# Performance work log

Hardware: AMD Instinct MI355X
Metric: run time of the kernel (lower is better)

## Reference

```python
import jax, jax.numpy as jnp
import numpy as np
from jax import lax

SEQ, B, F, L = 32, 32, 64, 256
OC = 128          # out_channels
K = 5
PAD = (K - 1) // 2
GROUPS = 4 * OC // 32  # GroupNorm groups = 16
EPS = 1e-5


def group_norm(x, w, b):
    # x: (B, C, L); normalize over each group's (C//G, L) slice
    bsz, c, l = x.shape
    xg = x.reshape(bsz, GROUPS, -1)
    mu = jnp.mean(xg, axis=-1, keepdims=True)
    var = jnp.var(xg, axis=-1, keepdims=True)
    xg = (xg - mu) * lax.rsqrt(var + EPS)
    return xg.reshape(bsz, c, l) * w[None, :, None] + b[None, :, None]


def setup_inputs() -> dict:
    key = jax.random.key(0)
    k1, k2, k3 = jax.random.split(key, 3)
    fan_in = (F + OC) * K
    return {
        "inputs": jax.random.normal(k1, (SEQ, B, F, L), dtype=jnp.float32),
        "conv_w": jax.random.normal(k2, (4 * OC, F + OC, K), dtype=jnp.float32) / np.sqrt(fan_in),
        "conv_b": jax.random.normal(k3, (4 * OC,), dtype=jnp.float32) * 0.01,
        "gn_w": jnp.ones((4 * OC,), dtype=jnp.float32),
        "gn_b": jnp.zeros((4 * OC,), dtype=jnp.float32),
    }


def reference(inputs, conv_w, conv_b, gn_w, gn_b):
    bsz, sub_len = inputs.shape[1], inputs.shape[3]
    hx0 = jnp.zeros((bsz, OC, sub_len), dtype=inputs.dtype)
    cx0 = jnp.zeros((bsz, OC, sub_len), dtype=inputs.dtype)

    def step(carry, x):
        hx, cx = carry
        combined = jnp.concatenate([x, hx], axis=1)  # (B, F+OC, L)
        gates = lax.conv_general_dilated(
            combined, conv_w, window_strides=(1,), padding=[(PAD, PAD)],
            dimension_numbers=("NCH", "OIH", "NCH"))
        gates = gates + conv_b[None, :, None]
        gates = group_norm(gates, gn_w, gn_b)
        i, f, g, o = jnp.split(gates, 4, axis=1)
        cy = jax.nn.sigmoid(f) * cx + jax.nn.sigmoid(i) * jnp.tanh(g)
        hy = jax.nn.sigmoid(o) * jnp.tanh(cy)
        return (hy, cy), hy

    (hy, cy), outputs = lax.scan(step, (hx0, cx0), inputs)
    return outputs, (hy, cy)
```

## Files before the change

kernel.cpp:

```cpp
#include <hip/hip_runtime.h>

typedef unsigned short u16;
typedef __attribute__((ext_vector_type(4))) float f32x4;
typedef __attribute__((ext_vector_type(8))) short s16x8;
typedef __attribute__((ext_vector_type(4))) int i32x4;

#define EPS 1e-5f

__device__ __forceinline__ u16 f2bf(float f) {
  unsigned u = __float_as_uint(f);
  return (u16)((u + 0x7fffu + ((u >> 16) & 1u)) >> 16);
}
__device__ __forceinline__ float sigm(float x) { return 1.0f / (1.0f + __expf(-x)); }
__device__ __forceinline__ float tanh_f(float x) {
  float e = __expf(-2.0f * fabsf(x));
  float r = (1.0f - e) / (1.0f + e);
  return copysignf(r, x);
}

__global__ __launch_bounds__(256) void k_wcvt(const float* __restrict__ w, u16* __restrict__ Wpk) {
  int idx = blockIdx.x * 256 + threadIdx.x;
  int f = idx >> 9, r = idx & 511;
  int lane = r >> 3, j = r & 7;
  int of = f & 31, tk = f >> 5;
  int kk = tk % 6, tap = tk / 6;
  int o = (of << 4) + (lane & 15);
  int c = (kk << 5) + ((lane >> 4) << 3) + j;
  Wpk[idx] = f2bf(w[(o * 192 + c) * 5 + tap]);
}

__global__ __launch_bounds__(256) void k_xtrans(const float* __restrict__ x, u16* __restrict__ xT) {
  int tb = blockIdx.x;
  int tid = threadIdx.x;
  __shared__ __align__(16) u16 ltile[256 * 72];
  const float* src = x + tb * (64 * 256);
  for (int it = 0; it < 64; ++it) {
    int idx = it * 256 + tid;
    int c = idx >> 8, l = idx & 255;
    ltile[l * 72 + c] = f2bf(src[idx]);
  }
  __syncthreads();
  char* dst = (char*)(xT + tb * 16896);
  i32x4 z = {0, 0, 0, 0};
  for (int i = tid; i < 2112; i += 256) {
    int r = i >> 3, ch = i & 7;
    i32x4 v = z;
    if (r >= 2 && r < 258) v = *(const i32x4*)(ltile + (r - 2) * 72 + ch * 8);
    *(i32x4*)(dst + r * 128 + ((ch * 16) ^ ((r & 7) << 4))) = v;
  }
}

__global__ void k_init(i32x4* __restrict__ hT, i32x4* __restrict__ cx) {
  int n = gridDim.x * blockDim.x;
  int tid = blockIdx.x * blockDim.x + threadIdx.x;
  i32x4 z = {0, 0, 0, 0};
  for (int i = tid; i < 270336; i += n) hT[i] = z;
  for (int i = tid; i < 262144; i += n) cx[i] = z;
}

__global__ __launch_bounds__(512, 2) void k_step(
    const u16* __restrict__ Wpk, const u16* __restrict__ xT, u16* __restrict__ hT,
    const float* __restrict__ cb, const float* __restrict__ gnw, const float* __restrict__ gnb,
    float* __restrict__ cx, float* __restrict__ out, int t) {
  int b = blockIdx.x >> 2, cs = blockIdx.x & 3;
  int tid = threadIdx.x, wave = tid >> 6, lane = tid & 63;
  int wrow = wave & 1, wcol = wave >> 1;

  __shared__ __align__(16) char ldsx[33792];
  __shared__ __align__(16) char ldsh[67584];
  __shared__ float red[8][4][2];
  __shared__ __align__(16) char hl[16384];

  const u16* hTr = hT + (t & 1) * 1081344;
  u16* hTw = hT + ((t + 1) & 1) * 1081344;

  {
    const i32x4* gx = (const i32x4*)(xT + ((t << 5) + b) * 16896);
    i32x4* lx = (i32x4*)ldsx;
    for (int i = tid; i < 2112; i += 512) lx[i] = gx[i];
    const i32x4* gh = (const i32x4*)(hTr + b * 33792);
    i32x4* lh = (i32x4*)ldsh;
    for (int i = tid; i < 4224; i += 512) lh[i] = gh[i];
  }
  __syncthreads();

  f32x4 zero4 = {0.f, 0.f, 0.f, 0.f};
  f32x4 acc[4][4];
  #pragma unroll
  for (int g = 0; g < 4; ++g)
    #pragma unroll
    for (int ni = 0; ni < 4; ++ni) acc[g][ni] = zero4;

  const s16x8* Wv = (const s16x8*)Wpk;
  int ofbase = (cs << 1) + wrow;
  int cgrp = (lane >> 4) << 4;

  for (int tap = 0; tap < 5; ++tap) {
    #pragma unroll
    for (int kk = 0; kk < 6; ++kk) {
      int fb = ((tap * 6 + kk) << 5) + ofbase;
      s16x8 av[4];
      #pragma unroll
      for (int g = 0; g < 4; ++g) av[g] = Wv[((fb + (g << 3)) << 6) + lane];
      s16x8 bv[4];
      #pragma unroll
      for (int ni = 0; ni < 4; ++ni) {
        int row = (wcol << 6) + (ni << 4) + (lane & 15) + tap;
        int sw = (row & 7) << 4;
        const char* p;
        if (kk < 2) p = ldsx + (row << 7) + (((kk << 6) + cgrp) ^ sw);
        else        p = ldsh + (row << 8) + ((((kk - 2) << 6) + cgrp) ^ sw);
        bv[ni] = *(const s16x8*)p;
      }
      #pragma unroll
      for (int g = 0; g < 4; ++g)
        #pragma unroll
        for (int ni = 0; ni < 4; ++ni)
          acc[g][ni] = __builtin_amdgcn_mfma_f32_16x16x32_bf16(av[g], bv[ni], acc[g][ni], 0, 0, 0);
    }
  }

  int ch16 = (lane >> 4) << 2;
  int cbase = (cs << 5) + (wrow << 4) + ch16;
  float sum[4], sq[4];
  #pragma unroll
  for (int g = 0; g < 4; ++g) {
    f32x4 bias = *(const f32x4*)(cb + (g << 7) + cbase);
    sum[g] = 0.f; sq[g] = 0.f;
    #pragma unroll
    for (int ni = 0; ni < 4; ++ni)
      #pragma unroll
      for (int r = 0; r < 4; ++r) {
        float v = acc[g][ni][r] + bias[r];
        acc[g][ni][r] = v;
        sum[g] += v; sq[g] += v * v;
      }
  }
  #pragma unroll
  for (int off = 1; off < 64; off <<= 1) {
    #pragma unroll
    for (int g = 0; g < 4; ++g) {
      sum[g] += __shfl_xor(sum[g], off);
      sq[g]  += __shfl_xor(sq[g], off);
    }
  }
  if (lane == 0) {
    #pragma unroll
    for (int g = 0; g < 4; ++g) { red[wave][g][0] = sum[g]; red[wave][g][1] = sq[g]; }
  }
  __syncthreads();

  const float inv = 1.0f / 8192.0f;
  float mu[4], rs[4];
  #pragma unroll
  for (int g = 0; g < 4; ++g) {
    float s = 0.f, q = 0.f;
    #pragma unroll
    for (int w = 0; w < 8; ++w) { s += red[w][g][0]; q += red[w][g][1]; }
    mu[g] = s * inv;
    rs[g] = rsqrtf(q * inv - mu[g] * mu[g] + EPS);
  }

  float w4[4][4], b4[4][4];
  #pragma unroll
  for (int g = 0; g < 4; ++g)
    #pragma unroll
    for (int r = 0; r < 4; ++r) {
      int c = (g << 7) + cbase + r;
      w4[g][r] = gnw[c]; b4[g][r] = gnb[c];
    }

  float* outp = out + (((t << 5) + b) << 15);
  int lhalf = lane & 15;
  #pragma unroll
  for (int ni = 0; ni < 4; ++ni) {
    int l = (wcol << 6) + (ni << 4) + lhalf;
    u16 hp[4];
    #pragma unroll
    for (int r = 0; r < 4; ++r) {
      int c = cbase + r;
      float vi = (acc[0][ni][r] - mu[0]) * rs[0] * w4[0][r] + b4[0][r];
      float vf = (acc[1][ni][r] - mu[1]) * rs[1] * w4[1][r] + b4[1][r];
      float vg = (acc[2][ni][r] - mu[2]) * rs[2] * w4[2][r] + b4[2][r];
      float vo = (acc[3][ni][r] - mu[3]) * rs[3] * w4[3][r] + b4[3][r];
      int cxi = (((b << 7) + c) << 8) + l;
      float cyv = sigm(vf) * cx[cxi] + sigm(vi) * tanh_f(vg);
      float hyv = sigm(vo) * tanh_f(cyv);
      cx[cxi] = cyv;
      outp[(c << 8) + l] = hyv;
      hp[r] = f2bf(hyv);
      if (t == 31) {
        out[33554432 + cxi] = hyv;
        out[34603008 + cxi] = cyv;
      }
    }
    int gran = (wrow << 5) + (ch16 << 1);
    *(unsigned long long*)(hl + (l << 6) + (gran ^ ((l & 3) << 4))) =
        *(const unsigned long long*)hp;
  }
  __syncthreads();

  char* dsth = (char*)(hTw + b * 33792);
  #pragma unroll
  for (int i = tid; i < 1024; i += 512) {
    int l = i >> 2, k = i & 3;
    int row = l + 2;
    i32x4 v = *(const i32x4*)(hl + (l << 6) + ((k << 4) ^ ((l & 3) << 4)));
    int c16 = (cs << 2) + k;
    *(i32x4*)(dsth + (row << 8) + ((c16 << 4) ^ ((row & 7) << 4))) = v;
  }
}

extern "C" void kernel_launch(void* const* d_in, const int* in_sizes, int n_in,
                              void* d_out, int out_size, void* d_ws, size_t ws_size,
                              hipStream_t stream) {
  const float* x  = (const float*)d_in[0];
  const float* cw = (const float*)d_in[1];
  const float* cb = (const float*)d_in[2];
  const float* gw = (const float*)d_in[3];
  const float* gb = (const float*)d_in[4];
  float* out = (float*)d_out;
  char* ws = (char*)d_ws;

  u16*   Wpk = (u16*)(ws);
  u16*   xT  = (u16*)(ws + 983040);
  u16*   hT  = (u16*)(ws + 35586048);
  float* cx  = (float*)(ws + 39911424);

  k_wcvt<<<1920, 256, 0, stream>>>(cw, Wpk);
  k_xtrans<<<1024, 256, 0, stream>>>(x, xT);
  k_init<<<512, 256, 0, stream>>>((i32x4*)hT, (i32x4*)cx);
  for (int t = 0; t < 32; ++t)
    k_step<<<128, 512, 0, stream>>>(Wpk, xT, hT, cb, gw, gb, cx, out, t);
}
```

Baseline: 821.1 us.

## Split each step's length axis across block pairs with flag-synchronised GroupNorm stats

Each (batch, channel-slice) block is split into two blocks covering half of the sequence length, so 256 blocks launch per step instead of 128. GroupNorm partial sums are exchanged between the paired blocks through global stats and a spin-wait on release/acquire flags. Weight tiles now stream through a 4-deep LDS ring using global_load_lds, and the x/h tiles use the same path. This adds more parallelism and async loads, but it risks deadlock if the paired blocks are not co-resident, and it adds a global sync on every step.

```diff
diff --git a/kernel.cpp b/kernel.cpp
--- a/kernel.cpp
+++ b/kernel.cpp
@@ -1,6 +1,7 @@
 #include <hip/hip_runtime.h>
 
 typedef unsigned short u16;
+typedef unsigned int u32;
 typedef __attribute__((ext_vector_type(4))) float f32x4;
 typedef __attribute__((ext_vector_type(8))) short s16x8;
 typedef __attribute__((ext_vector_type(4))) int i32x4;
@@ -16,6 +17,11 @@
   float e = __expf(-2.0f * fabsf(x));
   float r = (1.0f - e) / (1.0f + e);
   return copysignf(r, x);
+}
+__device__ __forceinline__ void gl_lds16(const void* g, void* l) {
+  __builtin_amdgcn_global_load_lds(
+      (const __attribute__((address_space(1))) u32*)g,
+      (__attribute__((address_space(3))) u32*)l, 16, 0, 0);
 }
 
 __global__ __launch_bounds__(256) void k_wcvt(const float* __restrict__ w, u16* __restrict__ Wpk) {
@@ -50,73 +56,80 @@
   }
 }
 
-__global__ void k_init(i32x4* __restrict__ hT, i32x4* __restrict__ cx) {
+__global__ void k_init(i32x4* __restrict__ hT, i32x4* __restrict__ cxv, i32x4* __restrict__ flg) {
   int n = gridDim.x * blockDim.x;
   int tid = blockIdx.x * blockDim.x + threadIdx.x;
   i32x4 z = {0, 0, 0, 0};
   for (int i = tid; i < 270336; i += n) hT[i] = z;
-  for (int i = tid; i < 262144; i += n) cx[i] = z;
-}
-
-__global__ __launch_bounds__(512, 2) void k_step(
+  for (int i = tid; i < 262144; i += n) cxv[i] = z;
+  for (int i = tid; i < 2048;   i += n) flg[i] = z;
+}
+
+__global__ __launch_bounds__(512) void k_step(
     const u16* __restrict__ Wpk, const u16* __restrict__ xT, u16* __restrict__ hT,
     const float* __restrict__ cb, const float* __restrict__ gnw, const float* __restrict__ gnb,
-    float* __restrict__ cx, float* __restrict__ out, int t) {
-  int b = blockIdx.x >> 2, cs = blockIdx.x & 3;
+    float* __restrict__ cx, float* __restrict__ out,
+    float* __restrict__ stats, int* __restrict__ flags, int t) {
+  int blk = blockIdx.x;
+  int b = blk >> 3, cs = (blk >> 1) & 3, lh = blk & 1;
   int tid = threadIdx.x, wave = tid >> 6, lane = tid & 63;
   int wrow = wave & 1, wcol = wave >> 1;
 
-  __shared__ __align__(16) char ldsx[33792];
-  __shared__ __align__(16) char ldsh[67584];
+  __shared__ __align__(16) char ldsx[16896];
+  __shared__ __align__(16) char ldsh[33792];
+  __shared__ __align__(16) char A_lds[4][8192];
+  __shared__ __align__(16) char hl[8192];
   __shared__ float red[8][4][2];
-  __shared__ __align__(16) char hl[16384];
+  __shared__ float smu[4], srs[4];
 
   const u16* hTr = hT + (t & 1) * 1081344;
   u16* hTw = hT + ((t + 1) & 1) * 1081344;
 
+  int ofw = ((wave >> 1) << 3) + (cs << 1) + (wave & 1);
+  gl_lds16(Wpk + ((ofw << 6) + lane) * 8, A_lds[0] + (wave << 10));
+  gl_lds16(Wpk + (((32 + ofw) << 6) + lane) * 8, A_lds[1] + (wave << 10));
   {
-    const i32x4* gx = (const i32x4*)(xT + ((t << 5) + b) * 16896);
-    i32x4* lx = (i32x4*)ldsx;
-    for (int i = tid; i < 2112; i += 512) lx[i] = gx[i];
-    const i32x4* gh = (const i32x4*)(hTr + b * 33792);
-    i32x4* lh = (i32x4*)ldsh;
-    for (int i = tid; i < 4224; i += 512) lh[i] = gh[i];
-  }
-  __syncthreads();
+    const char* gx = (const char*)(xT + ((t << 5) + b) * 16896 + (lh << 13));
+    for (int i = tid; i < 1056; i += 512)
+      gl_lds16(gx + (i << 4), ldsx + ((i >> 6) << 10));
+    const char* gh = (const char*)(hTr + b * 33792 + (lh << 14));
+    for (int i = tid; i < 2112; i += 512)
+      gl_lds16(gh + (i << 4), ldsh + ((i >> 6) << 10));
+  }
+  asm volatile("s_waitcnt vmcnt(0) lgkmcnt(0)" ::: "memory");
+  __builtin_amdgcn_s_barrier();
 
   f32x4 zero4 = {0.f, 0.f, 0.f, 0.f};
-  f32x4 acc[4][4];
-  #pragma unroll
-  for (int g = 0; g < 4; ++g)
-    #pragma unroll
-    for (int ni = 0; ni < 4; ++ni) acc[g][ni] = zero4;
-
-  const s16x8* Wv = (const s16x8*)Wpk;
-  int ofbase = (cs << 1) + wrow;
+  f32x4 acc[4][2];
+  #pragma unroll
+  for (int g = 0; g < 4; ++g) { acc[g][0] = zero4; acc[g][1] = zero4; }
   int cgrp = (lane >> 4) << 4;
 
-  for (int tap = 0; tap < 5; ++tap) {
-    #pragma unroll
-    for (int kk = 0; kk < 6; ++kk) {
-      int fb = ((tap * 6 + kk) << 5) + ofbase;
-      s16x8 av[4];
-      #pragma unroll
-      for (int g = 0; g < 4; ++g) av[g] = Wv[((fb + (g << 3)) << 6) + lane];
-      s16x8 bv[4];
-      #pragma unroll
-      for (int ni = 0; ni < 4; ++ni) {
-        int row = (wcol << 6) + (ni << 4) + (lane & 15) + tap;
-        int sw = (row & 7) << 4;
-        const char* p;
-        if (kk < 2) p = ldsx + (row << 7) + (((kk << 6) + cgrp) ^ sw);
-        else        p = ldsh + (row << 8) + ((((kk - 2) << 6) + cgrp) ^ sw);
-        bv[ni] = *(const s16x8*)p;
-      }
-      #pragma unroll
-      for (int g = 0; g < 4; ++g)
-        #pragma unroll
-        for (int ni = 0; ni < 4; ++ni)
-          acc[g][ni] = __builtin_amdgcn_mfma_f32_16x16x32_bf16(av[g], bv[ni], acc[g][ni], 0, 0, 0);
+  #pragma unroll
+  for (int c = 0; c < 30; ++c) {
+    int cn = (c + 2 < 30) ? (c + 2) : 29;
+    gl_lds16(Wpk + ((((cn << 5) + ofw) << 6) + lane) * 8, A_lds[(c + 2) & 3] + (wave << 10));
+    asm volatile("s_waitcnt vmcnt(2)" ::: "memory");
+    __builtin_amdgcn_s_barrier();
+    const char* Ab = A_lds[c & 3];
+    int tap = c / 6, kk = c % 6;
+    s16x8 av[4];
+    #pragma unroll
+    for (int g = 0; g < 4; ++g)
+      av[g] = *(const s16x8*)(Ab + (((g << 1) + wrow) << 10) + (lane << 4));
+    s16x8 bv[2];
+    #pragma unroll
+    for (int ni = 0; ni < 2; ++ni) {
+      int row = (wcol << 5) + (ni << 4) + (lane & 15) + tap;
+      int sw = (row & 7) << 4;
+      const char* p = (kk < 2) ? (ldsx + (row << 7) + (((kk << 6) + cgrp) ^ sw))
+                               : (ldsh + (row << 8) + ((((kk - 2) << 6) + cgrp) ^ sw));
+      bv[ni] = *(const s16x8*)p;
+    }
+    #pragma unroll
+    for (int g = 0; g < 4; ++g) {
+      acc[g][0] = __builtin_amdgcn_mfma_f32_16x16x32_bf16(av[g], bv[0], acc[g][0], 0, 0, 0);
+      acc[g][1] = __builtin_amdgcn_mfma_f32_16x16x32_bf16(av[g], bv[1], acc[g][1], 0, 0, 0);
     }
   }
 
@@ -128,7 +141,7 @@
     f32x4 bias = *(const f32x4*)(cb + (g << 7) + cbase);
     sum[g] = 0.f; sq[g] = 0.f;
     #pragma unroll
-    for (int ni = 0; ni < 4; ++ni)
+    for (int ni = 0; ni < 2; ++ni)
       #pragma unroll
       for (int r = 0; r < 4; ++r) {
         float v = acc[g][ni][r] + bias[r];
@@ -150,39 +163,58 @@
   }
   __syncthreads();
 
-  const float inv = 1.0f / 8192.0f;
-  float mu[4], rs[4];
+  int slot = (((t << 5) + b) << 3) + (cs << 1) + lh;
+  if (tid == 0) {
+    #pragma unroll
+    for (int g = 0; g < 4; ++g) {
+      float s = 0.f, q = 0.f;
+      #pragma unroll
+      for (int w = 0; w < 8; ++w) { s += red[w][g][0]; q += red[w][g][1]; }
+      __hip_atomic_store(&stats[(slot << 3) + (g << 1)], s, __ATOMIC_RELAXED, __HIP_MEMORY_SCOPE_AGENT);
+      __hip_atomic_store(&stats[(slot << 3) + (g << 1) + 1], q, __ATOMIC_RELAXED, __HIP_MEMORY_SCOPE_AGENT);
+    }
+    __hip_atomic_store(&flags[slot], 1, __ATOMIC_RELEASE, __HIP_MEMORY_SCOPE_AGENT);
+    while (__hip_atomic_load(&flags[slot ^ 1], __ATOMIC_ACQUIRE, __HIP_MEMORY_SCOPE_AGENT) == 0) {}
+  }
+  __syncthreads();
+  if (tid < 4) {
+    int base = (slot >> 1) << 4;
+    float s = __hip_atomic_load(&stats[base + (tid << 1)], __ATOMIC_RELAXED, __HIP_MEMORY_SCOPE_AGENT)
+            + __hip_atomic_load(&stats[base + 8 + (tid << 1)], __ATOMIC_RELAXED, __HIP_MEMORY_SCOPE_AGENT);
+    float q = __hip_atomic_load(&stats[base + (tid << 1) + 1], __ATOMIC_RELAXED, __HIP_MEMORY_SCOPE_AGENT)
+            + __hip_atomic_load(&stats[base + 8 + (tid << 1) + 1], __ATOMIC_RELAXED, __HIP_MEMORY_SCOPE_AGENT);
+    const float inv = 1.0f / 8192.0f;
+    float m = s * inv;
+    smu[tid] = m;
+    srs[tid] = rsqrtf(q * inv - m * m + EPS);
+  }
+  __syncthreads();
+
+  float w4[4][4], b4[4][4], muv[4], rsv[4];
   #pragma unroll
   for (int g = 0; g < 4; ++g) {
-    float s = 0.f, q = 0.f;
-    #pragma unroll
-    for (int w = 0; w < 8; ++w) { s += red[w][g][0]; q += red[w][g][1]; }
-    mu[g] = s * inv;
-    rs[g] = rsqrtf(q * inv - mu[g] * mu[g] + EPS);
-  }
-
-  float w4[4][4], b4[4][4];
-  #pragma unroll
-  for (int g = 0; g < 4; ++g)
+    muv[g] = smu[g]; rsv[g] = srs[g];
     #pragma unroll
     for (int r = 0; r < 4; ++r) {
       int c = (g << 7) + cbase + r;
       w4[g][r] = gnw[c]; b4[g][r] = gnb[c];
     }
-
+  }
   float* outp = out + (((t << 5) + b) << 15);
   int lhalf = lane & 15;
-  #pragma unroll
-  for (int ni = 0; ni < 4; ++ni) {
-    int l = (wcol << 6) + (ni << 4) + lhalf;
+  int gran = (wrow << 5) + (ch16 << 1);
+  #pragma unroll
+  for (int ni = 0; ni < 2; ++ni) {
+    int ll = (wcol << 5) + (ni << 4) + lhalf;
+    int l = (lh << 7) + ll;
     u16 hp[4];
     #pragma unroll
     for (int r = 0; r < 4; ++r) {
       int c = cbase + r;
-      float vi = (acc[0][ni][r] - mu[0]) * rs[0] * w4[0][r] + b4[0][r];
-      float vf = (acc[1][ni][r] - mu[1]) * rs[1] * w4[1][r] + b4[1][r];
-      float vg = (acc[2][ni][r] - mu[2]) * rs[2] * w4[2][r] + b4[2][r];
-      float vo = (acc[3][ni][r] - mu[3]) * rs[3] * w4[3][r] + b4[3][r];
+      float vi = (acc[0][ni][r] - muv[0]) * rsv[0] * w4[0][r] + b4[0][r];
+      float vf = (acc[1][ni][r] - muv[1]) * rsv[1] * w4[1][r] + b4[1][r];
+      float vg = (acc[2][ni][r] - muv[2]) * rsv[2] * w4[2][r] + b4[2][r];
+      float vo = (acc[3][ni][r] - muv[3]) * rsv[3] * w4[3][r] + b4[3][r];
       int cxi = (((b << 7) + c) << 8) + l;
       float cyv = sigm(vf) * cx[cxi] + sigm(vi) * tanh_f(vg);
       float hyv = sigm(vo) * tanh_f(cyv);
@@ -194,20 +226,17 @@
         out[34603008 + cxi] = cyv;
       }
     }
-    int gran = (wrow << 5) + (ch16 << 1);
-    *(unsigned long long*)(hl + (l << 6) + (gran ^ ((l & 3) << 4))) =
+    *(unsigned long long*)(hl + (ll << 6) + (gran ^ ((ll & 3) << 4))) =
         *(const unsigned long long*)hp;
   }
   __syncthreads();
 
-  char* dsth = (char*)(hTw + b * 33792);
-  #pragma unroll
-  for (int i = tid; i < 1024; i += 512) {
-    int l = i >> 2, k = i & 3;
-    int row = l + 2;
-    i32x4 v = *(const i32x4*)(hl + (l << 6) + ((k << 4) ^ ((l & 3) << 4)));
-    int c16 = (cs << 2) + k;
-    *(i32x4*)(dsth + (row << 8) + ((c16 << 4) ^ ((row & 7) << 4))) = v;
+  {
+    int ll = tid >> 2, k = tid & 3;
+    int row = (lh << 7) + ll + 2;
+    i32x4 v = *(const i32x4*)(hl + (ll << 6) + ((k << 4) ^ ((ll & 3) << 4)));
+    char* dsth = (char*)hTw + b * 67584 + (row << 8) + ((((cs << 2) + k) << 4) ^ ((row & 7) << 4));
+    *(i32x4*)dsth = v;
   }
 }
 
@@ -222,14 +251,16 @@
   float* out = (float*)d_out;
   char* ws = (char*)d_ws;
 
-  u16*   Wpk = (u16*)(ws);
-  u16*   xT  = (u16*)(ws + 983040);
-  u16*   hT  = (u16*)(ws + 35586048);
-  float* cx  = (float*)(ws + 39911424);
+  u16*   Wpk   = (u16*)(ws);
+  u16*   xT    = (u16*)(ws + 983040);
+  u16*   hT    = (u16*)(ws + 35586048);
+  float* cx    = (float*)(ws + 39911424);
+  float* stats = (float*)(ws + 44105728);
+  int*   flags = (int*)(ws + 44367872);
 
   k_wcvt<<<1920, 256, 0, stream>>>(cw, Wpk);
   k_xtrans<<<1024, 256, 0, stream>>>(x, xT);
-  k_init<<<512, 256, 0, stream>>>((i32x4*)hT, (i32x4*)cx);
+  k_init<<<512, 256, 0, stream>>>((i32x4*)hT, (i32x4*)cx, (i32x4*)flags);
   for (int t = 0; t < 32; ++t)
-    k_step<<<128, 512, 0, stream>>>(Wpk, xT, hT, cb, gw, gb, cx, out, t);
-}
+    k_step<<<256, 512, 0, stream>>>(Wpk, xT, hT, cb, gw, gb, cx, out, stats, flags, t);
+}
```

Result: faster. 699.9 us (-14.8%).
